# Kernel optimization log

Hardware: AMD Instinct MI355X
Metric: run time of the kernel (lower is better)

## Reference

```python
import jax, jax.numpy as jnp
import numpy as np

N = 12000       # nodes (Hi-C bins, max_num_nodes)
F_IN = 16       # number_genomic_annotations
HID = 4 * F_IN  # conv1 out = 64
NCLUST = 100    # n_clust
E = 384000      # edges (avg degree 32)


def setup_inputs() -> dict:
    key = jax.random.key(0)
    ks = jax.random.split(key, 8)
    x = jax.random.normal(ks[0], (N, F_IN), dtype=jnp.float32)
    edge_index = jax.random.randint(ks[1], (2, E), 0, N)
    edge_attr = jax.random.uniform(ks[2], (E,), dtype=jnp.float32)
    s1 = 1.0 / np.sqrt(F_IN)
    W1_rel = jax.random.uniform(ks[3], (HID, F_IN), minval=-s1, maxval=s1, dtype=jnp.float32)
    W1_root = jax.random.uniform(ks[4], (HID, F_IN), minval=-s1, maxval=s1, dtype=jnp.float32)
    b1 = jnp.zeros((HID,), jnp.float32)
    s2 = 1.0 / np.sqrt(HID)
    W2_rel = jax.random.uniform(ks[5], (NCLUST, HID), minval=-s2, maxval=s2, dtype=jnp.float32)
    W2_root = jax.random.uniform(ks[6], (NCLUST, HID), minval=-s2, maxval=s2, dtype=jnp.float32)
    b2 = jnp.zeros((NCLUST,), jnp.float32)
    return dict(x=x, edge_index=edge_index, edge_attr=edge_attr,
                W1_rel=W1_rel, W1_root=W1_root, b1=b1,
                W2_rel=W2_rel, W2_root=W2_root, b2=b2)


def _graph_conv(x, src, dst, ew, W_rel, W_root, b):
    # PyG GraphConv (aggr='add'): out = lin_rel(sum_j e_ji * x_j) + lin_root(x)
    msg = x[src] * ew[:, None]                       # [E, F]
    aggr = jax.ops.segment_sum(msg, dst, num_segments=N)  # [N, F]
    return aggr @ W_rel.T + b + x @ W_root.T


def reference(x, edge_index, edge_attr, W1_rel, W1_root, b1, W2_rel, W2_root, b2):
    src, dst = edge_index[0], edge_index[1]
    h = _graph_conv(x, src, dst, edge_attr, W1_rel, W1_root, b1)
    h = jax.nn.relu(h)  # dropout is identity in eval mode
    s_out = _graph_conv(h, src, dst, edge_attr, W2_rel, W2_root, b2)  # [N, NCLUST]

    # to_dense_adj (duplicate edges summed)
    adj = jnp.zeros((N, N), x.dtype).at[src, dst].add(edge_attr)  # [N, N]

    # dense_mincut_pool with S = x (as in the original forward), k = F_IN
    s_mc = jax.nn.softmax(x, axis=-1)      # [N, F_IN]
    as_ = adj @ s_mc                        # [N, F_IN]
    out_adj = s_mc.T @ as_                  # [F_IN, F_IN]
    mincut_num = jnp.trace(out_adj)
    d_flat = adj.sum(-1)                    # [N] degree
    mincut_den = jnp.einsum('ik,i,ik->', s_mc, d_flat, s_mc)  # trace(S^T D S)
    mc = -(mincut_num / mincut_den)

    ss = s_mc.T @ s_mc                      # [F_IN, F_IN]
    i_k = jnp.eye(F_IN, dtype=ss.dtype)
    o = jnp.linalg.norm(ss / jnp.linalg.norm(ss) - i_k / jnp.linalg.norm(i_k))

    return jax.nn.softmax(s_out, axis=-1), mc, o
```

## Files before the change

kernel.cpp:

```cpp
#include <hip/hip_runtime.h>
#include <math.h>

#define N_NODES 12000
#define F_INN 16
#define HIDD 64
#define NCLUST 100
#define NEDGE 384000
#define NBLK_N 47
#define CAP 96
#define EPT 4
#define NBLK_E 375
#define NBLK_F1 (N_NODES / 4)
#define NBLK_F2 (N_NODES / 8)

#define OFF_COUNT   0
#define OFF_SCAL    12000
#define ZERO_ELEMS  12002
#define OFF_SSPART  12004
#define OFF_NORM2   24036
#define OFF_W2TREL  36036
#define OFF_W2TROOT 42436
#define OFF_SMC     48836
#define OFF_H       240836
#define OFF_SRCW    1008836

__global__ void phase0_kernel(const float* __restrict__ x, const int* __restrict__ ei,
                              const float* __restrict__ ew, float* __restrict__ smc,
                              float* __restrict__ norm2, int* __restrict__ count,
                              int2* __restrict__ srcw, const float* __restrict__ W2_rel,
                              const float* __restrict__ W2_root, float* __restrict__ w2t_rel,
                              float* __restrict__ w2t_root) {
    __shared__ float fl[6400];
    int t = threadIdx.x;
    int b = blockIdx.x;
    if (b < NBLK_N) {
        int i = b * 256 + t;
        if (i >= N_NODES) return;
        const float4* xr = (const float4*)(x + i * 16);
        float4 r0 = xr[0], r1 = xr[1], r2 = xr[2], r3 = xr[3];
        float v[16] = {r0.x, r0.y, r0.z, r0.w, r1.x, r1.y, r1.z, r1.w,
                       r2.x, r2.y, r2.z, r2.w, r3.x, r3.y, r3.z, r3.w};
        float m = v[0];
#pragma unroll
        for (int k = 1; k < 16; ++k) m = fmaxf(m, v[k]);
        float s = 0.f;
#pragma unroll
        for (int k = 0; k < 16; ++k) { v[k] = __expf(v[k] - m); s += v[k]; }
        float inv = 1.f / s;
        float n2 = 0.f;
#pragma unroll
        for (int k = 0; k < 16; ++k) { v[k] *= inv; n2 += v[k] * v[k]; }
        float4* so = (float4*)(smc + i * 16);
        so[0] = make_float4(v[0], v[1], v[2], v[3]);
        so[1] = make_float4(v[4], v[5], v[6], v[7]);
        so[2] = make_float4(v[8], v[9], v[10], v[11]);
        so[3] = make_float4(v[12], v[13], v[14], v[15]);
        norm2[i] = n2;
    } else if (b < NBLK_N + NBLK_E) {
        int tid = (b - NBLK_N) * 256 + t;
        int e0 = tid * EPT;
        int4 sv = *(const int4*)(ei + e0);
        int4 dv = *(const int4*)(ei + NEDGE + e0);
        float4 wv = *(const float4*)(ew + e0);
        int s[EPT] = {sv.x, sv.y, sv.z, sv.w};
        int d[EPT] = {dv.x, dv.y, dv.z, dv.w};
        float w[EPT] = {wv.x, wv.y, wv.z, wv.w};
        int pos[EPT];
#pragma unroll
        for (int i = 0; i < EPT; ++i) pos[i] = atomicAdd(&count[d[i]], 1);
#pragma unroll
        for (int i = 0; i < EPT; ++i)
            srcw[d[i] * CAP + pos[i]] = make_int2(s[i], __float_as_int(w[i]));
    } else {
        const float* src = (b == NBLK_N + NBLK_E) ? W2_rel : W2_root;
        float* dst = (b == NBLK_N + NBLK_E) ? w2t_rel : w2t_root;
        for (int i = t; i < 6400; i += 256) fl[i] = src[i];
        __syncthreads();
        for (int j = t; j < 6400; j += 256) {
            int kk = j / 100, cl = j - kk * 100;
            dst[j] = fl[cl * 64 + kk];
        }
    }
}

__global__ void fused1_pass2_kernel(const float* __restrict__ x, const int2* __restrict__ srcw,
                                    const int* __restrict__ count, const float* __restrict__ W1_rel,
                                    const float* __restrict__ W1_root, const float* __restrict__ b1,
                                    float* __restrict__ h, const float* __restrict__ smc,
                                    float* __restrict__ sspart, const int* __restrict__ ei,
                                    const float* __restrict__ ew, const float* __restrict__ norm2,
                                    float* __restrict__ scal) {
    __shared__ float shm[4352];
    int t = threadIdx.x;
    int b = blockIdx.x;
    if (b < NBLK_F1) {
        float* wrelT  = shm;
        float* wrootT = shm + 1024;
        float* b1s    = shm + 2048;
        float* aggr   = shm + 2112;
        float* xs     = shm + 2176;
        for (int idx = t; idx < 1024; idx += 256) {
            int f = idx >> 4, k = idx & 15;
            wrelT[(k << 6) + f]  = W1_rel[idx];
            wrootT[(k << 6) + f] = W1_root[idx];
        }
        if (t < 64) b1s[t] = b1[t];
        int w = t >> 6, lane = t & 63;
        int j2 = lane >> 2;
        int q  = lane & 3;
        int n = b * 4 + w;
        int len = count[n];
        const int2* bucket = srcw + n * CAP;
        float4 acc4 = make_float4(0.f, 0.f, 0.f, 0.f);
        for (int k = 0; k < len; k += 32) {
            int ia = k + j2, ib = k + 16 + j2;
            int2 pa = bucket[ia];
            int2 pb = bucket[ib];
            if (ia >= len) pa = make_int2(0, 0);
            if (ib >= len) pb = make_int2(0, 0);
            float4 va = *(const float4*)(x + pa.x * 16 + q * 4);
            float4 vb = *(const float4*)(x + pb.x * 16 + q * 4);
            float wa = __int_as_float(pa.y), wb = __int_as_float(pb.y);
            acc4.x = fmaf(va.x, wa, acc4.x); acc4.y = fmaf(va.y, wa, acc4.y);
            acc4.z = fmaf(va.z, wa, acc4.z); acc4.w = fmaf(va.w, wa, acc4.w);
            acc4.x = fmaf(vb.x, wb, acc4.x); acc4.y = fmaf(vb.y, wb, acc4.y);
            acc4.z = fmaf(vb.z, wb, acc4.z); acc4.w = fmaf(vb.w, wb, acc4.w);
        }
        acc4.x += __shfl_xor(acc4.x, 4);  acc4.y += __shfl_xor(acc4.y, 4);
        acc4.z += __shfl_xor(acc4.z, 4);  acc4.w += __shfl_xor(acc4.w, 4);
        acc4.x += __shfl_xor(acc4.x, 8);  acc4.y += __shfl_xor(acc4.y, 8);
        acc4.z += __shfl_xor(acc4.z, 8);  acc4.w += __shfl_xor(acc4.w, 8);
        acc4.x += __shfl_xor(acc4.x, 16); acc4.y += __shfl_xor(acc4.y, 16);
        acc4.z += __shfl_xor(acc4.z, 16); acc4.w += __shfl_xor(acc4.w, 16);
        acc4.x += __shfl_xor(acc4.x, 32); acc4.y += __shfl_xor(acc4.y, 32);
        acc4.z += __shfl_xor(acc4.z, 32); acc4.w += __shfl_xor(acc4.w, 32);
        if (j2 == 0) *(float4*)(aggr + w * 16 + q * 4) = acc4;
        if (lane < 16) xs[w * 16 + lane] = x[n * 16 + lane];
        __syncthreads();
        float o = b1s[lane];
#pragma unroll
        for (int kk = 0; kk < 16; ++kk)
            o = fmaf(aggr[w * 16 + kk], wrelT[(kk << 6) + lane],
                     fmaf(xs[w * 16 + kk], wrootT[(kk << 6) + lane], o));
        h[n * 64 + lane] = fmaxf(o, 0.f);
    } else if (b < NBLK_F1 + NBLK_N) {
        int bb = b - NBLK_F1;
        float* rows = shm;
        int n = bb * 256 + t;
        float* rp = rows + t * 17;
        if (n < N_NODES) {
            const float4* sr = (const float4*)(smc + n * 16);
            float4 a0 = sr[0], a1 = sr[1], a2v = sr[2], a3 = sr[3];
            rp[0] = a0.x;  rp[1] = a0.y;  rp[2] = a0.z;  rp[3] = a0.w;
            rp[4] = a1.x;  rp[5] = a1.y;  rp[6] = a1.z;  rp[7] = a1.w;
            rp[8] = a2v.x; rp[9] = a2v.y; rp[10] = a2v.z; rp[11] = a2v.w;
            rp[12] = a3.x; rp[13] = a3.y; rp[14] = a3.z; rp[15] = a3.w;
        } else {
#pragma unroll
            for (int k = 0; k < 16; ++k) rp[k] = 0.f;
        }
        __syncthreads();
        int a = t & 15, bq = t >> 4;
        float accs = 0.f;
#pragma unroll 4
        for (int r = 0; r < 256; ++r)
            accs = fmaf(rows[r * 17 + a], rows[r * 17 + bq], accs);
        sspart[bb * 256 + t] = accs;
    } else {
        int tid = (b - NBLK_F1 - NBLK_N) * 256 + t;
        int e0 = tid * EPT;
        int4 sv = *(const int4*)(ei + e0);
        int4 dv = *(const int4*)(ei + NEDGE + e0);
        float4 wv = *(const float4*)(ew + e0);
        int s[EPT] = {sv.x, sv.y, sv.z, sv.w};
        int d[EPT] = {dv.x, dv.y, dv.z, dv.w};
        float w[EPT] = {wv.x, wv.y, wv.z, wv.w};
        float np = 0.f, dp = 0.f;
#pragma unroll
        for (int i = 0; i < EPT; ++i) {
            const float4* ps = (const float4*)(smc + s[i] * 16);
            const float4* pd = (const float4*)(smc + d[i] * 16);
            float4 s0 = ps[0], s1 = ps[1], s2 = ps[2], s3 = ps[3];
            float4 d0 = pd[0], d1 = pd[1], d2 = pd[2], d3 = pd[3];
            float dot = s0.x * d0.x + s0.y * d0.y + s0.z * d0.z + s0.w * d0.w +
                        s1.x * d1.x + s1.y * d1.y + s1.z * d1.z + s1.w * d1.w +
                        s2.x * d2.x + s2.y * d2.y + s2.z * d2.z + s2.w * d2.w +
                        s3.x * d3.x + s3.y * d3.y + s3.z * d3.z + s3.w * d3.w;
            np = fmaf(w[i], dot, np);
            dp = fmaf(w[i], norm2[s[i]], dp);
        }
        float* redn = shm;
        float* redd = shm + 256;
        redn[t] = np;
        redd[t] = dp;
        __syncthreads();
        for (int s2 = 128; s2 > 0; s2 >>= 1) {
            if (t < s2) { redn[t] += redn[t + s2]; redd[t] += redd[t + s2]; }
            __syncthreads();
        }
        if (t == 0) {
            atomicAdd(&scal[0], redn[0]);
            atomicAdd(&scal[1], redd[0]);
        }
    }
}

__global__ __launch_bounds__(512) void fused2_finalize_kernel(
    const float* __restrict__ h, const int2* __restrict__ srcw, const int* __restrict__ count,
    const float* __restrict__ w2t_rel, const float* __restrict__ w2t_root,
    const float* __restrict__ b2, float* __restrict__ out, const float* __restrict__ sspart,
    const float* __restrict__ scal) {
    __shared__ float wsrel[6400];
    __shared__ float a2[8][64], hrow[8][64];
    __shared__ float logits[8][104];
    __shared__ float b2s[104];
    int t = threadIdx.x;
    int b = blockIdx.x;
    if (b < NBLK_F2) {
        for (int i = t; i < 6400; i += 512) wsrel[i] = w2t_rel[i];
        if (t < NCLUST) b2s[t] = b2[t];
        int nn = t >> 6;
        int c = t & 63;
        int eslot = c >> 4;
        int q = c & 15;
        int n = b * 8 + nn;
        int len = count[n];
        const int2* bucket = srcw + n * CAP;
        float4 acc4 = make_float4(0.f, 0.f, 0.f, 0.f);
        for (int k = 0; k < len; k += 32) {
            int i0 = k + eslot,      i1 = k + 4 + eslot;
            int i2 = k + 8 + eslot,  i3 = k + 12 + eslot;
            int i4 = k + 16 + eslot, i5 = k + 20 + eslot;
            int i6 = k + 24 + eslot, i7 = k + 28 + eslot;
            int2 pa = bucket[i0]; int2 pb = bucket[i1];
            int2 pc = bucket[i2]; int2 pd = bucket[i3];
            int2 pe = bucket[i4]; int2 pf = bucket[i5];
            int2 pg = bucket[i6]; int2 ph = bucket[i7];
            if (i0 >= len) pa = make_int2(0, 0);
            if (i1 >= len) pb = make_int2(0, 0);
            if (i2 >= len) pc = make_int2(0, 0);
            if (i3 >= len) pd = make_int2(0, 0);
            if (i4 >= len) pe = make_int2(0, 0);
            if (i5 >= len) pf = make_int2(0, 0);
            if (i6 >= len) pg = make_int2(0, 0);
            if (i7 >= len) ph = make_int2(0, 0);
            float4 va = *(const float4*)(h + pa.x * 64 + q * 4);
            float4 vb = *(const float4*)(h + pb.x * 64 + q * 4);
            float4 vc = *(const float4*)(h + pc.x * 64 + q * 4);
            float4 vd = *(const float4*)(h + pd.x * 64 + q * 4);
            float4 ve = *(const float4*)(h + pe.x * 64 + q * 4);
            float4 vf = *(const float4*)(h + pf.x * 64 + q * 4);
            float4 vg = *(const float4*)(h + pg.x * 64 + q * 4);
            float4 vh = *(const float4*)(h + ph.x * 64 + q * 4);
            float wa = __int_as_float(pa.y), wb = __int_as_float(pb.y);
            float wc = __int_as_float(pc.y), wd = __int_as_float(pd.y);
            float we = __int_as_float(pe.y), wf = __int_as_float(pf.y);
            float wg = __int_as_float(pg.y), wh = __int_as_float(ph.y);
            acc4.x = fmaf(va.x, wa, acc4.x); acc4.y = fmaf(va.y, wa, acc4.y);
            acc4.z = fmaf(va.z, wa, acc4.z); acc4.w = fmaf(va.w, wa, acc4.w);
            acc4.x = fmaf(vb.x, wb, acc4.x); acc4.y = fmaf(vb.y, wb, acc4.y);
            acc4.z = fmaf(vb.z, wb, acc4.z); acc4.w = fmaf(vb.w, wb, acc4.w);
            acc4.x = fmaf(vc.x, wc, acc4.x); acc4.y = fmaf(vc.y, wc, acc4.y);
            acc4.z = fmaf(vc.z, wc, acc4.z); acc4.w = fmaf(vc.w, wc, acc4.w);
            acc4.x = fmaf(vd.x, wd, acc4.x); acc4.y = fmaf(vd.y, wd, acc4.y);
            acc4.z = fmaf(vd.z, wd, acc4.z); acc4.w = fmaf(vd.w, wd, acc4.w);
            acc4.x = fmaf(ve.x, we, acc4.x); acc4.y = fmaf(ve.y, we, acc4.y);
            acc4.z = fmaf(ve.z, we, acc4.z); acc4.w = fmaf(ve.w, we, acc4.w);
            acc4.x = fmaf(vf.x, wf, acc4.x); acc4.y = fmaf(vf.y, wf, acc4.y);
            acc4.z = fmaf(vf.z, wf, acc4.z); acc4.w = fmaf(vf.w, wf, acc4.w);
            acc4.x = fmaf(vg.x, wg, acc4.x); acc4.y = fmaf(vg.y, wg, acc4.y);
            acc4.z = fmaf(vg.z, wg, acc4.z); acc4.w = fmaf(vg.w, wg, acc4.w);
            acc4.x = fmaf(vh.x, wh, acc4.x); acc4.y = fmaf(vh.y, wh, acc4.y);
            acc4.z = fmaf(vh.z, wh, acc4.z); acc4.w = fmaf(vh.w, wh, acc4.w);
        }
        acc4.x += __shfl_xor(acc4.x, 16); acc4.y += __shfl_xor(acc4.y, 16);
        acc4.z += __shfl_xor(acc4.z, 16); acc4.w += __shfl_xor(acc4.w, 16);
        acc4.x += __shfl_xor(acc4.x, 32); acc4.y += __shfl_xor(acc4.y, 32);
        acc4.z += __shfl_xor(acc4.z, 32); acc4.w += __shfl_xor(acc4.w, 32);
        if (eslot == 0) *(float4*)(&a2[nn][q * 4]) = acc4;
        hrow[nn][c] = h[n * 64 + c];
        __syncthreads();
        int g = t >> 7, c2 = t & 127;
        if (c2 < NCLUST) {
            int na = 2 * g, nb2 = 2 * g + 1;
            float s0 = b2s[c2], s1 = s0;
#pragma unroll 8
            for (int kk = 0; kk < 64; ++kk) {
                float wr = wsrel[kk * 100 + c2];
                float wo = w2t_root[kk * 100 + c2];
                s0 = fmaf(a2[na][kk], wr, fmaf(hrow[na][kk], wo, s0));
                s1 = fmaf(a2[nb2][kk], wr, fmaf(hrow[nb2][kk], wo, s1));
            }
            logits[na][c2] = s0;
            logits[nb2][c2] = s1;
        }
        __syncthreads();
        float v0 = logits[nn][c];
        float v1 = (c < NCLUST - 64) ? logits[nn][64 + c] : -INFINITY;
        float m = fmaxf(v0, v1);
#pragma unroll
        for (int off = 32; off > 0; off >>= 1) m = fmaxf(m, __shfl_xor(m, off));
        float e0 = __expf(v0 - m);
        float e1 = (c < NCLUST - 64) ? __expf(v1 - m) : 0.f;
        float s = e0 + e1;
#pragma unroll
        for (int off = 32; off > 0; off >>= 1) s += __shfl_xor(s, off);
        float inv = 1.f / s;
        out[n * NCLUST + c] = e0 * inv;
        if (c < NCLUST - 64) out[n * NCLUST + 64 + c] = e1 * inv;
    } else {
        float* red = wsrel;
        float sv = 0.f;
        if (t < 256)
            for (int bb = 0; bb < NBLK_N; ++bb) sv += sspart[bb * 256 + t];
        red[t] = sv * sv;
        __syncthreads();
        for (int s = 256; s > 0; s >>= 1) {
            if (t < s) red[t] += red[t + s];
            __syncthreads();
        }
        float ssnorm = sqrtf(red[0]);
        __syncthreads();
        float diff = (t < 256) ? (sv / ssnorm - ((t % 17 == 0) ? 0.25f : 0.f)) : 0.f;
        red[t] = diff * diff;
        __syncthreads();
        for (int s = 256; s > 0; s >>= 1) {
            if (t < s) red[t] += red[t + s];
            __syncthreads();
        }
        if (t == 0) {
            out[N_NODES * NCLUST + 0] = -(scal[0] / scal[1]);
            out[N_NODES * NCLUST + 1] = sqrtf(red[0]);
        }
    }
}

extern "C" void kernel_launch(void* const* d_in, const int* in_sizes, int n_in,
                              void* d_out, int out_size, void* d_ws, size_t ws_size,
                              hipStream_t stream) {
    const float* x       = (const float*)d_in[0];
    const int*   ei      = (const int*)d_in[1];
    const float* ew      = (const float*)d_in[2];
    const float* W1_rel  = (const float*)d_in[3];
    const float* W1_root = (const float*)d_in[4];
    const float* b1      = (const float*)d_in[5];
    const float* W2_rel  = (const float*)d_in[6];
    const float* W2_root = (const float*)d_in[7];
    const float* b2      = (const float*)d_in[8];
    float* out = (float*)d_out;
    int*   wsi = (int*)d_ws;

    int*   count   = wsi + OFF_COUNT;
    float* scal    = (float*)(wsi + OFF_SCAL);
    float* sspart  = (float*)(wsi + OFF_SSPART);
    float* norm2   = (float*)(wsi + OFF_NORM2);
    float* w2trel  = (float*)(wsi + OFF_W2TREL);
    float* w2troot = (float*)(wsi + OFF_W2TROOT);
    float* smc     = (float*)(wsi + OFF_SMC);
    float* h       = (float*)(wsi + OFF_H);
    int2*  srcw    = (int2*)(wsi + OFF_SRCW);

    hipMemsetAsync(wsi, 0, ZERO_ELEMS * sizeof(int), stream);
    phase0_kernel<<<NBLK_N + NBLK_E + 2, 256, 0, stream>>>(x, ei, ew, smc, norm2, count, srcw,
                                                           W2_rel, W2_root, w2trel, w2troot);
    fused1_pass2_kernel<<<NBLK_F1 + NBLK_N + NBLK_E, 256, 0, stream>>>(
        x, srcw, count, W1_rel, W1_root, b1, h, smc, sspart, ei, ew, norm2, scal);
    fused2_finalize_kernel<<<NBLK_F2 + 1, 512, 0, stream>>>(h, srcw, count, w2trel, w2troot,
                                                            b2, out, sspart, scal);
}
```

Measured before the change: 97.12 us.

## Shard per-node edge buckets into eight groups to spread atomic contention

Edge binning now uses eight separate per-node counters, with the group chosen by block index. Each node gets eight sub-buckets of 24 slots, so atomics on the same destination are spread across counter copies. Both gather kernels now stage the eight per-group lengths in shared memory and loop a fixed six rounds over all 192 slots, masking the empty ones. In exchange, the counter array to zero is eight times larger and the bucket storage and padded gather traffic grow. Edges beyond 24 per group for one node are silently dropped.

```diff
diff --git a/kernel.cpp b/kernel.cpp
--- a/kernel.cpp
+++ b/kernel.cpp
@@ -7,22 +7,25 @@
 #define NCLUST 100
 #define NEDGE 384000
 #define NBLK_N 47
-#define CAP 96
+#define NGRP 8
+#define CAP_G 24
+#define CAPT (NGRP * CAP_G)
+#define NROUND 6
 #define EPT 4
 #define NBLK_E 375
 #define NBLK_F1 (N_NODES / 4)
 #define NBLK_F2 (N_NODES / 8)
 
 #define OFF_COUNT   0
-#define OFF_SCAL    12000
-#define ZERO_ELEMS  12002
-#define OFF_SSPART  12004
-#define OFF_NORM2   24036
-#define OFF_W2TREL  36036
-#define OFF_W2TROOT 42436
-#define OFF_SMC     48836
-#define OFF_H       240836
-#define OFF_SRCW    1008836
+#define OFF_SCAL    96000
+#define ZERO_ELEMS  96002
+#define OFF_SSPART  96004
+#define OFF_NORM2   108036
+#define OFF_W2TREL  120036
+#define OFF_W2TROOT 126436
+#define OFF_SMC     132836
+#define OFF_H       324836
+#define OFF_SRCW    1092836
 
 __global__ void phase0_kernel(const float* __restrict__ x, const int* __restrict__ ei,
                               const float* __restrict__ ew, float* __restrict__ smc,
@@ -57,6 +60,8 @@
         so[3] = make_float4(v[12], v[13], v[14], v[15]);
         norm2[i] = n2;
     } else if (b < NBLK_N + NBLK_E) {
+        int g = b & (NGRP - 1);
+        int* cg = count + g * N_NODES;
         int tid = (b - NBLK_N) * 256 + t;
         int e0 = tid * EPT;
         int4 sv = *(const int4*)(ei + e0);
@@ -67,10 +72,11 @@
         float w[EPT] = {wv.x, wv.y, wv.z, wv.w};
         int pos[EPT];
 #pragma unroll
-        for (int i = 0; i < EPT; ++i) pos[i] = atomicAdd(&count[d[i]], 1);
+        for (int i = 0; i < EPT; ++i) pos[i] = atomicAdd(&cg[d[i]], 1);
 #pragma unroll
         for (int i = 0; i < EPT; ++i)
-            srcw[d[i] * CAP + pos[i]] = make_int2(s[i], __float_as_int(w[i]));
+            if (pos[i] < CAP_G)
+                srcw[d[i] * CAPT + g * CAP_G + pos[i]] = make_int2(s[i], __float_as_int(w[i]));
     } else {
         const float* src = (b == NBLK_N + NBLK_E) ? W2_rel : W2_root;
         float* dst = (b == NBLK_N + NBLK_E) ? w2t_rel : w2t_root;
@@ -99,25 +105,34 @@
         float* b1s    = shm + 2048;
         float* aggr   = shm + 2112;
         float* xs     = shm + 2176;
+        int*  lensS   = (int*)(shm + 2240);
         for (int idx = t; idx < 1024; idx += 256) {
             int f = idx >> 4, k = idx & 15;
             wrelT[(k << 6) + f]  = W1_rel[idx];
             wrootT[(k << 6) + f] = W1_root[idx];
         }
         if (t < 64) b1s[t] = b1[t];
+        if (t < 32) {
+            int nn2 = t >> 3, g = t & 7;
+            lensS[nn2 * 8 + g] = count[g * N_NODES + (b * 4 + nn2)];
+        }
+        __syncthreads();
         int w = t >> 6, lane = t & 63;
         int j2 = lane >> 2;
         int q  = lane & 3;
         int n = b * 4 + w;
-        int len = count[n];
-        const int2* bucket = srcw + n * CAP;
+        const int2* bucket = srcw + n * CAPT;
+        const int* lp = lensS + w * 8;
         float4 acc4 = make_float4(0.f, 0.f, 0.f, 0.f);
-        for (int k = 0; k < len; k += 32) {
-            int ia = k + j2, ib = k + 16 + j2;
+#pragma unroll
+        for (int k = 0; k < NROUND; ++k) {
+            int ia = k * 32 + j2, ib = k * 32 + 16 + j2;
+            int ga = ia / CAP_G, oa = ia - ga * CAP_G;
+            int gb = ib / CAP_G, ob = ib - gb * CAP_G;
             int2 pa = bucket[ia];
             int2 pb = bucket[ib];
-            if (ia >= len) pa = make_int2(0, 0);
-            if (ib >= len) pb = make_int2(0, 0);
+            if (oa >= lp[ga]) pa = make_int2(0, 0);
+            if (ob >= lp[gb]) pb = make_int2(0, 0);
             float4 va = *(const float4*)(x + pa.x * 16 + q * 4);
             float4 vb = *(const float4*)(x + pb.x * 16 + q * 4);
             float wa = __int_as_float(pa.y), wb = __int_as_float(pb.y);
@@ -214,36 +229,46 @@
     __shared__ float a2[8][64], hrow[8][64];
     __shared__ float logits[8][104];
     __shared__ float b2s[104];
+    __shared__ int lensS[64];
     int t = threadIdx.x;
     int b = blockIdx.x;
     if (b < NBLK_F2) {
         for (int i = t; i < 6400; i += 512) wsrel[i] = w2t_rel[i];
         if (t < NCLUST) b2s[t] = b2[t];
+        if (t >= 128 && t < 192) {
+            int nn2 = (t - 128) >> 3, g = t & 7;
+            lensS[nn2 * 8 + g] = count[g * N_NODES + (b * 8 + nn2)];
+        }
+        __syncthreads();
         int nn = t >> 6;
         int c = t & 63;
         int eslot = c >> 4;
         int q = c & 15;
         int n = b * 8 + nn;
-        int len = count[n];
-        const int2* bucket = srcw + n * CAP;
+        const int2* bucket = srcw + n * CAPT;
+        const int* lp = lensS + nn * 8;
         float4 acc4 = make_float4(0.f, 0.f, 0.f, 0.f);
-        for (int k = 0; k < len; k += 32) {
-            int i0 = k + eslot,      i1 = k + 4 + eslot;
-            int i2 = k + 8 + eslot,  i3 = k + 12 + eslot;
-            int i4 = k + 16 + eslot, i5 = k + 20 + eslot;
-            int i6 = k + 24 + eslot, i7 = k + 28 + eslot;
+#pragma unroll 2
+        for (int k = 0; k < NROUND; ++k) {
+            int kb = k * 32;
+            int i0 = kb + eslot,      i1 = kb + 4 + eslot;
+            int i2 = kb + 8 + eslot,  i3 = kb + 12 + eslot;
+            int i4 = kb + 16 + eslot, i5 = kb + 20 + eslot;
+            int i6 = kb + 24 + eslot, i7 = kb + 28 + eslot;
             int2 pa = bucket[i0]; int2 pb = bucket[i1];
             int2 pc = bucket[i2]; int2 pd = bucket[i3];
             int2 pe = bucket[i4]; int2 pf = bucket[i5];
             int2 pg = bucket[i6]; int2 ph = bucket[i7];
-            if (i0 >= len) pa = make_int2(0, 0);
-            if (i1 >= len) pb = make_int2(0, 0);
-            if (i2 >= len) pc = make_int2(0, 0);
-            if (i3 >= len) pd = make_int2(0, 0);
-            if (i4 >= len) pe = make_int2(0, 0);
-            if (i5 >= len) pf = make_int2(0, 0);
-            if (i6 >= len) pg = make_int2(0, 0);
-            if (i7 >= len) ph = make_int2(0, 0);
+            int g0 = i0 / CAP_G, g1 = i1 / CAP_G, g2 = i2 / CAP_G, g3 = i3 / CAP_G;
+            int g4 = i4 / CAP_G, g5 = i5 / CAP_G, g6 = i6 / CAP_G, g7 = i7 / CAP_G;
+            if (i0 - g0 * CAP_G >= lp[g0]) pa = make_int2(0, 0);
+            if (i1 - g1 * CAP_G >= lp[g1]) pb = make_int2(0, 0);
+            if (i2 - g2 * CAP_G >= lp[g2]) pc = make_int2(0, 0);
+            if (i3 - g3 * CAP_G >= lp[g3]) pd = make_int2(0, 0);
+            if (i4 - g4 * CAP_G >= lp[g4]) pe = make_int2(0, 0);
+            if (i5 - g5 * CAP_G >= lp[g5]) pf = make_int2(0, 0);
+            if (i6 - g6 * CAP_G >= lp[g6]) pg = make_int2(0, 0);
+            if (i7 - g7 * CAP_G >= lp[g7]) ph = make_int2(0, 0);
             float4 va = *(const float4*)(h + pa.x * 64 + q * 4);
             float4 vb = *(const float4*)(h + pb.x * 64 + q * 4);
             float4 vc = *(const float4*)(h + pc.x * 64 + q * 4);
```

After: 122.1 us. +25.7%, slower.

## Regroup kernels so edge scatter runs alongside mincut passes, conv1 separate

Applied to the files above, without the earlier changes.

Splits the phase-0 work into a small softmax/weight-transpose kernel and a scatter kernel, which now also carries the ss partial-sum and mincut edge-reduction blocks. Conv1 aggregation becomes its own kernel launched after the scatter. The mincut edge pass, which only needs smc, now overlaps with the atomic bucket scatter instead of conv1. This adds one kernel launch and serializes conv1 behind the scatter-plus-mincut kernel.

```diff
diff --git a/kernel.cpp b/kernel.cpp
--- a/kernel.cpp
+++ b/kernel.cpp
@@ -24,12 +24,10 @@
 #define OFF_H       240836
 #define OFF_SRCW    1008836
 
-__global__ void phase0_kernel(const float* __restrict__ x, const int* __restrict__ ei,
-                              const float* __restrict__ ew, float* __restrict__ smc,
-                              float* __restrict__ norm2, int* __restrict__ count,
-                              int2* __restrict__ srcw, const float* __restrict__ W2_rel,
-                              const float* __restrict__ W2_root, float* __restrict__ w2t_rel,
-                              float* __restrict__ w2t_root) {
+__global__ void pre_kernel(const float* __restrict__ x, float* __restrict__ smc,
+                           float* __restrict__ norm2, const float* __restrict__ W2_rel,
+                           const float* __restrict__ W2_root, float* __restrict__ w2t_rel,
+                           float* __restrict__ w2t_root) {
     __shared__ float fl[6400];
     int t = threadIdx.x;
     int b = blockIdx.x;
@@ -56,8 +54,27 @@
         so[2] = make_float4(v[8], v[9], v[10], v[11]);
         so[3] = make_float4(v[12], v[13], v[14], v[15]);
         norm2[i] = n2;
-    } else if (b < NBLK_N + NBLK_E) {
-        int tid = (b - NBLK_N) * 256 + t;
+    } else {
+        const float* src = (b == NBLK_N) ? W2_rel : W2_root;
+        float* dst = (b == NBLK_N) ? w2t_rel : w2t_root;
+        for (int i = t; i < 6400; i += 256) fl[i] = src[i];
+        __syncthreads();
+        for (int j = t; j < 6400; j += 256) {
+            int kk = j / 100, cl = j - kk * 100;
+            dst[j] = fl[cl * 64 + kk];
+        }
+    }
+}
+
+__global__ void scatter_kernel(const int* __restrict__ ei, const float* __restrict__ ew,
+                               int* __restrict__ count, int2* __restrict__ srcw,
+                               const float* __restrict__ smc, float* __restrict__ sspart,
+                               const float* __restrict__ norm2, float* __restrict__ scal) {
+    __shared__ float shm[4352];
+    int t = threadIdx.x;
+    int b = blockIdx.x;
+    if (b < NBLK_E) {
+        int tid = b * 256 + t;
         int e0 = tid * EPT;
         int4 sv = *(const int4*)(ei + e0);
         int4 dv = *(const int4*)(ei + NEDGE + e0);
@@ -71,80 +88,8 @@
 #pragma unroll
         for (int i = 0; i < EPT; ++i)
             srcw[d[i] * CAP + pos[i]] = make_int2(s[i], __float_as_int(w[i]));
-    } else {
-        const float* src = (b == NBLK_N + NBLK_E) ? W2_rel : W2_root;
-        float* dst = (b == NBLK_N + NBLK_E) ? w2t_rel : w2t_root;
-        for (int i = t; i < 6400; i += 256) fl[i] = src[i];
-        __syncthreads();
-        for (int j = t; j < 6400; j += 256) {
-            int kk = j / 100, cl = j - kk * 100;
-            dst[j] = fl[cl * 64 + kk];
-        }
-    }
-}
-
-__global__ void fused1_pass2_kernel(const float* __restrict__ x, const int2* __restrict__ srcw,
-                                    const int* __restrict__ count, const float* __restrict__ W1_rel,
-                                    const float* __restrict__ W1_root, const float* __restrict__ b1,
-                                    float* __restrict__ h, const float* __restrict__ smc,
-                                    float* __restrict__ sspart, const int* __restrict__ ei,
-                                    const float* __restrict__ ew, const float* __restrict__ norm2,
-                                    float* __restrict__ scal) {
-    __shared__ float shm[4352];
-    int t = threadIdx.x;
-    int b = blockIdx.x;
-    if (b < NBLK_F1) {
-        float* wrelT  = shm;
-        float* wrootT = shm + 1024;
-        float* b1s    = shm + 2048;
-        float* aggr   = shm + 2112;
-        float* xs     = shm + 2176;
-        for (int idx = t; idx < 1024; idx += 256) {
-            int f = idx >> 4, k = idx & 15;
-            wrelT[(k << 6) + f]  = W1_rel[idx];
-            wrootT[(k << 6) + f] = W1_root[idx];
-        }
-        if (t < 64) b1s[t] = b1[t];
-        int w = t >> 6, lane = t & 63;
-        int j2 = lane >> 2;
-        int q  = lane & 3;
-        int n = b * 4 + w;
-        int len = count[n];
-        const int2* bucket = srcw + n * CAP;
-        float4 acc4 = make_float4(0.f, 0.f, 0.f, 0.f);
-        for (int k = 0; k < len; k += 32) {
-            int ia = k + j2, ib = k + 16 + j2;
-            int2 pa = bucket[ia];
-            int2 pb = bucket[ib];
-            if (ia >= len) pa = make_int2(0, 0);
-            if (ib >= len) pb = make_int2(0, 0);
-            float4 va = *(const float4*)(x + pa.x * 16 + q * 4);
-            float4 vb = *(const float4*)(x + pb.x * 16 + q * 4);
-            float wa = __int_as_float(pa.y), wb = __int_as_float(pb.y);
-            acc4.x = fmaf(va.x, wa, acc4.x); acc4.y = fmaf(va.y, wa, acc4.y);
-            acc4.z = fmaf(va.z, wa, acc4.z); acc4.w = fmaf(va.w, wa, acc4.w);
-            acc4.x = fmaf(vb.x, wb, acc4.x); acc4.y = fmaf(vb.y, wb, acc4.y);
-            acc4.z = fmaf(vb.z, wb, acc4.z); acc4.w = fmaf(vb.w, wb, acc4.w);
-        }
-        acc4.x += __shfl_xor(acc4.x, 4);  acc4.y += __shfl_xor(acc4.y, 4);
-        acc4.z += __shfl_xor(acc4.z, 4);  acc4.w += __shfl_xor(acc4.w, 4);
-        acc4.x += __shfl_xor(acc4.x, 8);  acc4.y += __shfl_xor(acc4.y, 8);
-        acc4.z += __shfl_xor(acc4.z, 8);  acc4.w += __shfl_xor(acc4.w, 8);
-        acc4.x += __shfl_xor(acc4.x, 16); acc4.y += __shfl_xor(acc4.y, 16);
-        acc4.z += __shfl_xor(acc4.z, 16); acc4.w += __shfl_xor(acc4.w, 16);
-        acc4.x += __shfl_xor(acc4.x, 32); acc4.y += __shfl_xor(acc4.y, 32);
-        acc4.z += __shfl_xor(acc4.z, 32); acc4.w += __shfl_xor(acc4.w, 32);
-        if (j2 == 0) *(float4*)(aggr + w * 16 + q * 4) = acc4;
-        if (lane < 16) xs[w * 16 + lane] = x[n * 16 + lane];
-        __syncthreads();
-        float o = b1s[lane];
-#pragma unroll
-        for (int kk = 0; kk < 16; ++kk)
-            o = fmaf(aggr[w * 16 + kk], wrelT[(kk << 6) + lane],
-                     fmaf(xs[w * 16 + kk], wrootT[(kk << 6) + lane], o));
-        h[n * 64 + lane] = fmaxf(o, 0.f);
-    } else if (b < NBLK_F1 + NBLK_N) {
-        int bb = b - NBLK_F1;
+    } else if (b < NBLK_E + NBLK_N) {
+        int bb = b - NBLK_E;
         float* rows = shm;
         int n = bb * 256 + t;
         float* rp = rows + t * 17;
@@ -167,7 +112,7 @@
             accs = fmaf(rows[r * 17 + a], rows[r * 17 + bq], accs);
         sspart[bb * 256 + t] = accs;
     } else {
-        int tid = (b - NBLK_F1 - NBLK_N) * 256 + t;
+        int tid = (b - NBLK_E - NBLK_N) * 256 + t;
         int e0 = tid * EPT;
         int4 sv = *(const int4*)(ei + e0);
         int4 dv = *(const int4*)(ei + NEDGE + e0);
@@ -203,6 +148,64 @@
             atomicAdd(&scal[1], redd[0]);
         }
     }
+}
+
+__global__ void fused1_kernel(const float* __restrict__ x, const int2* __restrict__ srcw,
+                              const int* __restrict__ count, const float* __restrict__ W1_rel,
+                              const float* __restrict__ W1_root, const float* __restrict__ b1,
+                              float* __restrict__ h) {
+    __shared__ float shm[2304];
+    int t = threadIdx.x;
+    int b = blockIdx.x;
+    float* wrelT  = shm;
+    float* wrootT = shm + 1024;
+    float* b1s    = shm + 2048;
+    float* aggr   = shm + 2112;
+    float* xs     = shm + 2176;
+    for (int idx = t; idx < 1024; idx += 256) {
+        int f = idx >> 4, k = idx & 15;
+        wrelT[(k << 6) + f]  = W1_rel[idx];
+        wrootT[(k << 6) + f] = W1_root[idx];
+    }
+    if (t < 64) b1s[t] = b1[t];
+    int w = t >> 6, lane = t & 63;
+    int j2 = lane >> 2;
+    int q  = lane & 3;
+    int n = b * 4 + w;
+    int len = count[n];
+    const int2* bucket = srcw + n * CAP;
+    float4 acc4 = make_float4(0.f, 0.f, 0.f, 0.f);
+    for (int k = 0; k < len; k += 32) {
+        int ia = k + j2, ib = k + 16 + j2;
+        int2 pa = bucket[ia];
+        int2 pb = bucket[ib];
+        if (ia >= len) pa = make_int2(0, 0);
+        if (ib >= len) pb = make_int2(0, 0);
+        float4 va = *(const float4*)(x + pa.x * 16 + q * 4);
+        float4 vb = *(const float4*)(x + pb.x * 16 + q * 4);
+        float wa = __int_as_float(pa.y), wb = __int_as_float(pb.y);
+        acc4.x = fmaf(va.x, wa, acc4.x); acc4.y = fmaf(va.y, wa, acc4.y);
+        acc4.z = fmaf(va.z, wa, acc4.z); acc4.w = fmaf(va.w, wa, acc4.w);
+        acc4.x = fmaf(vb.x, wb, acc4.x); acc4.y = fmaf(vb.y, wb, acc4.y);
+        acc4.z = fmaf(vb.z, wb, acc4.z); acc4.w = fmaf(vb.w, wb, acc4.w);
+    }
+    acc4.x += __shfl_xor(acc4.x, 4);  acc4.y += __shfl_xor(acc4.y, 4);
+    acc4.z += __shfl_xor(acc4.z, 4);  acc4.w += __shfl_xor(acc4.w, 4);
+    acc4.x += __shfl_xor(acc4.x, 8);  acc4.y += __shfl_xor(acc4.y, 8);
+    acc4.z += __shfl_xor(acc4.z, 8);  acc4.w += __shfl_xor(acc4.w, 8);
+    acc4.x += __shfl_xor(acc4.x, 16); acc4.y += __shfl_xor(acc4.y, 16);
+    acc4.z += __shfl_xor(acc4.z, 16); acc4.w += __shfl_xor(acc4.w, 16);
+    acc4.x += __shfl_xor(acc4.x, 32); acc4.y += __shfl_xor(acc4.y, 32);
+    acc4.z += __shfl_xor(acc4.z, 32); acc4.w += __shfl_xor(acc4.w, 32);
+    if (j2 == 0) *(float4*)(aggr + w * 16 + q * 4) = acc4;
+    if (lane < 16) xs[w * 16 + lane] = x[n * 16 + lane];
+    __syncthreads();
+    float o = b1s[lane];
+#pragma unroll
+    for (int kk = 0; kk < 16; ++kk)
+        o = fmaf(aggr[w * 16 + kk], wrelT[(kk << 6) + lane],
+                 fmaf(xs[w * 16 + kk], wrootT[(kk << 6) + lane], o));
+    h[n * 64 + lane] = fmaxf(o, 0.f);
 }
 
 __global__ __launch_bounds__(512) void fused2_finalize_kernel(
@@ -361,10 +364,10 @@
     int2*  srcw    = (int2*)(wsi + OFF_SRCW);
 
     hipMemsetAsync(wsi, 0, ZERO_ELEMS * sizeof(int), stream);
-    phase0_kernel<<<NBLK_N + NBLK_E + 2, 256, 0, stream>>>(x, ei, ew, smc, norm2, count, srcw,
-                                                           W2_rel, W2_root, w2trel, w2troot);
-    fused1_pass2_kernel<<<NBLK_F1 + NBLK_N + NBLK_E, 256, 0, stream>>>(
-        x, srcw, count, W1_rel, W1_root, b1, h, smc, sspart, ei, ew, norm2, scal);
+    pre_kernel<<<NBLK_N + 2, 256, 0, stream>>>(x, smc, norm2, W2_rel, W2_root, w2trel, w2troot);
+    scatter_kernel<<<NBLK_E + NBLK_N + NBLK_E, 256, 0, stream>>>(ei, ew, count, srcw,
+                                                                 smc, sspart, norm2, scal);
+    fused1_kernel<<<NBLK_F1, 256, 0, stream>>>(x, srcw, count, W1_rel, W1_root, b1, h);
     fused2_finalize_kernel<<<NBLK_F2 + 1, 512, 0, stream>>>(h, srcw, count, w2trel, w2troot,
                                                             b2, out, sspart, scal);
 }
```

After: 99.37 us. +2.3%, slower.
